# Optimization experiments

Hardware: AMD Instinct MI355X
Metric: run time of the kernel (lower is better)

Reference implementation:

```python
import math
import jax, jax.numpy as jnp
import numpy as np

B, S, H = 8, 1024, 1024
NH = 16
HD = H // NH  # 64


def setup_inputs() -> dict:
    key = jax.random.key(0)
    k1, k2, k3, k4 = jax.random.split(key, 4)
    hidden_states = jax.random.normal(k1, (B, S, H), dtype=jnp.float32)
    attention_mask = jax.random.randint(k2, (B, 1, 1, S), 0, 2, dtype=jnp.int32)
    w_qkv = jax.random.normal(k3, (H, 3 * H), dtype=jnp.float32) * (1.0 / math.sqrt(H))
    b_qkv = jax.random.normal(k4, (3 * H,), dtype=jnp.float32) * 0.02
    return {"hidden_states": hidden_states, "attention_mask": attention_mask,
            "w_qkv": w_qkv, "b_qkv": b_qkv}


def reference(hidden_states, attention_mask, w_qkv, b_qkv):
    b, s, _ = hidden_states.shape
    # fused QKV projection: [b, s, 3H]
    qkv = jnp.einsum('bsh,hk->bsk', hidden_states, w_qkv) + b_qkv
    # view (b, s, nh, 3*hd) -> permute -> chunk last dim (per-head q|k|v layout)
    qkv = qkv.reshape(b, s, NH, 3, HD)
    qkv = jnp.transpose(qkv, (0, 2, 1, 3, 4))      # [b, nh, s, 3, hd]
    q, k, v = qkv[..., 0, :], qkv[..., 1, :], qkv[..., 2, :]
    # raw scores, then FusedScaleMaskSoftmax semantics: scale * scores, mask, fp32 softmax
    scores = jnp.einsum('bhqd,bhkd->bhqk', q, k)
    scale = math.sqrt(HD)  # module passes sqrt(head_dim) as multiplicative scale
    scores = scores.astype(jnp.float32) * scale
    mask = attention_mask != 0                     # nonzero -> masked (padding)
    scores = jnp.where(mask, jnp.float32(-10000.0), scores)
    probs = jax.nn.softmax(scores, axis=-1).astype(hidden_states.dtype)
    # dropout prob = 0 -> identity
    context = jnp.einsum('bhqk,bhkd->bhqd', probs, v)
    context = jnp.transpose(context, (0, 2, 1, 3)).reshape(b, s, NH * HD)
    return context
```

## Files before the change

kernel.cpp:

```cpp
#include <hip/hip_runtime.h>
#include <math.h>

#define Bdim 8
#define Sdim 1024
#define Hdim 1024
#define NHd 16
#define HDd 64
#define N3H 3072

#define Q_OFF   0u
#define K_OFF   16777216u
#define V_OFF   33554432u
#define WH_OFF  41943040u
#define WL_OFF  45088768u
#define AHI_OFF 0u
#define ALO_OFF 8388608u

typedef __bf16 bf16x8 __attribute__((ext_vector_type(8)));
typedef float  f32x4  __attribute__((ext_vector_type(4)));

__device__ __forceinline__ unsigned short f2bf(float x) {
  unsigned b = __builtin_bit_cast(unsigned, x);
  return (unsigned short)((b + 0x7FFFu + ((b >> 16) & 1u)) >> 16);
}
__device__ __forceinline__ float bf2f(unsigned short h) {
  unsigned b = ((unsigned)h) << 16;
  return __builtin_bit_cast(float, b);
}
__device__ __forceinline__ void split_hl(float v, unsigned short& h, unsigned short& l) {
  h = f2bf(v);
  l = f2bf(v - bf2f(h));
}
__device__ __forceinline__ void async16(void* lds, const void* g) {
  __builtin_amdgcn_global_load_lds((const __attribute__((address_space(1))) unsigned int*)g,
                                   (__attribute__((address_space(3))) unsigned int*)lds, 16, 0, 0);
}

__global__ __launch_bounds__(256) void convert_AW(
    const float* __restrict__ A, const float* __restrict__ W,
    unsigned short* __restrict__ aout, unsigned short* __restrict__ ws)
{
  __shared__ float T[64][65];
  const int tid = threadIdx.x;
  int bid = blockIdx.x;
  if (bid < 4096) {
    size_t i = ((size_t)bid * 256 + tid) * 8;
    float4 a0 = *(const float4*)&A[i];
    float4 a1 = *(const float4*)&A[i + 4];
    float av[8] = {a0.x, a0.y, a0.z, a0.w, a1.x, a1.y, a1.z, a1.w};
    unsigned short h[8], l[8];
    #pragma unroll
    for (int j = 0; j < 8; ++j) split_hl(av[j], h[j], l[j]);
    *(uint4*)&aout[AHI_OFF + i] = *(uint4*)h;
    *(uint4*)&aout[ALO_OFF + i] = *(uint4*)l;
    return;
  }
  bid -= 4096;
  const int n0 = (bid % (N3H / 64)) * 64;
  const int k0 = (bid / (N3H / 64)) * 64;
  #pragma unroll
  for (int r = 0; r < 4; ++r) {
    int k = r * 16 + (tid >> 4);
    int n = (tid & 15) * 4;
    float4 v = *(const float4*)&W[(size_t)(k0 + k) * N3H + n0 + n];
    T[k][n + 0] = v.x; T[k][n + 1] = v.y; T[k][n + 2] = v.z; T[k][n + 3] = v.w;
  }
  __syncthreads();
  int n = tid >> 2;
  int kl = (tid & 3) * 16;
  unsigned short h[16], l[16];
  #pragma unroll
  for (int i = 0; i < 16; ++i) split_hl(T[kl + i][n], h[i], l[i]);
  size_t base = (size_t)(n0 + n) * 1024 + k0 + kl;
  *(uint4*)&ws[WH_OFF + base]     = *(uint4*)&h[0];
  *(uint4*)&ws[WH_OFF + base + 8] = *(uint4*)&h[8];
  *(uint4*)&ws[WL_OFF + base]     = *(uint4*)&l[0];
  *(uint4*)&ws[WL_OFF + base + 8] = *(uint4*)&l[8];
}

__global__ __launch_bounds__(256, 2) void qkv_mfma(
    const unsigned short* __restrict__ ao,
    const unsigned short* __restrict__ ws,
    const float* __restrict__ bias,
    unsigned short* __restrict__ wso)
{
  __shared__ unsigned short sA[2][128 * 32];
  __shared__ unsigned short sB[2][128 * 32];

  const int tid  = threadIdx.x;
  const int wave = tid >> 6;
  const int lane = tid & 63;
  const int l16  = lane & 15;
  const int quad = lane >> 4;

  const int n0 = blockIdx.x * 128;
  const int m0 = blockIdx.y * 128;
  const int wm = (wave >> 1) * 64;
  const int wn = (wave & 1) * 64;

  const unsigned short* Ah = ao + AHI_OFF;
  const unsigned short* Al = ao + ALO_OFF;
  const unsigned short* Wh = ws + WH_OFF;
  const unsigned short* Wl = ws + WL_OFF;

  f32x4 acc[4][4];
  #pragma unroll
  for (int i = 0; i < 4; ++i)
    #pragma unroll
    for (int j = 0; j < 4; ++j) acc[i][j] = (f32x4){0.f, 0.f, 0.f, 0.f};

  for (int kt = 0; kt < 1024; kt += 32) {
    __syncthreads();
    #pragma unroll
    for (int r = 0; r < 2; ++r) {
      int chunk = r * 256 + tid;
      int row = chunk >> 2;
      int c8  = (chunk & 3) << 3;
      int ldsoff = (r * 256 + wave * 64) * 8;
      async16(&sA[0][ldsoff], &Ah[(size_t)(m0 + row) * 1024 + kt + c8]);
      async16(&sA[1][ldsoff], &Al[(size_t)(m0 + row) * 1024 + kt + c8]);
      async16(&sB[0][ldsoff], &Wh[(size_t)(n0 + row) * 1024 + kt + c8]);
      async16(&sB[1][ldsoff], &Wl[(size_t)(n0 + row) * 1024 + kt + c8]);
    }
    __syncthreads();

    bf16x8 af[4][2], bf[4][2];
    #pragma unroll
    for (int i = 0; i < 4; ++i) {
      int row = wm + i * 16 + l16;
      af[i][0] = *(const bf16x8*)&sA[0][row * 32 + quad * 8];
      af[i][1] = *(const bf16x8*)&sA[1][row * 32 + quad * 8];
    }
    #pragma unroll
    for (int j = 0; j < 4; ++j) {
      int row = wn + j * 16 + l16;
      bf[j][0] = *(const bf16x8*)&sB[0][row * 32 + quad * 8];
      bf[j][1] = *(const bf16x8*)&sB[1][row * 32 + quad * 8];
    }
    #pragma unroll
    for (int i = 0; i < 4; ++i)
      #pragma unroll
      for (int j = 0; j < 4; ++j) {
        acc[i][j] = __builtin_amdgcn_mfma_f32_16x16x32_bf16(af[i][0], bf[j][0], acc[i][j], 0, 0, 0);
        acc[i][j] = __builtin_amdgcn_mfma_f32_16x16x32_bf16(af[i][1], bf[j][0], acc[i][j], 0, 0, 0);
        acc[i][j] = __builtin_amdgcn_mfma_f32_16x16x32_bf16(af[i][0], bf[j][1], acc[i][j], 0, 0, 0);
      }
  }

  const int ncol0 = n0 + wn;
  const int which = (ncol0 >> 6) % 3;
  const int head  = ncol0 / 192;
  const int mrow0 = m0 + wm;
  const int bb = mrow0 >> 10;
  const int sb = mrow0 & 1023;
  const int bh = bb * NHd + head;

  float bs[4];
  #pragma unroll
  for (int j = 0; j < 4; ++j) bs[j] = bias[ncol0 + j * 16 + l16];

  if (which == 0) {
    unsigned short* dst = wso + Q_OFF + ((size_t)bh * Sdim + sb) * 128;
    #pragma unroll
    for (int i = 0; i < 4; ++i)
      #pragma unroll
      for (int j = 0; j < 4; ++j) {
        int d = j * 16 + l16;
        #pragma unroll
        for (int r = 0; r < 4; ++r) {
          int s = i * 16 + quad * 4 + r;
          unsigned short h, l;
          split_hl(acc[i][j][r] + bs[j], h, l);
          dst[(size_t)s * 128 + d]      = h;
          dst[(size_t)s * 128 + 64 + d] = l;
        }
      }
  } else if (which == 1) {
    unsigned short* dst = wso + K_OFF + (size_t)bh * 131072 + (size_t)(sb >> 6) * 8192;
    #pragma unroll
    for (int i = 0; i < 4; ++i)
      #pragma unroll
      for (int j = 0; j < 4; ++j) {
        int c = j * 16 + l16;
        #pragma unroll
        for (int r = 0; r < 4; ++r) {
          int sp = i * 16 + quad * 4 + r;
          int idx = ((((sp >> 4) * 4 + (c >> 5)) * 64 + ((c >> 3) & 3) * 16 + (sp & 15)) << 3) + (c & 7);
          unsigned short h, l;
          split_hl(acc[i][j][r] + bs[j], h, l);
          dst[idx]        = h;
          dst[idx + 1024] = l;
        }
      }
  } else {
    unsigned short* dst = wso + V_OFF + (size_t)bh * 65536 + (size_t)(sb >> 6) * 4096;
    #pragma unroll
    for (int i = 0; i < 4; ++i)
      #pragma unroll
      for (int j = 0; j < 4; ++j) {
        int dr = j * 16 + l16;
        int ky = i * 16 + quad * 4;
        int idx = ((((dr >> 4) * 2 + (ky >> 5)) * 64 + ((ky >> 3) & 3) * 16 + (dr & 15)) << 3) + (ky & 7);
        unsigned short p[4];
        #pragma unroll
        for (int r = 0; r < 4; ++r) p[r] = f2bf(acc[i][j][r] + bs[j]);
        *(uint2*)&dst[idx] = *(uint2*)p;
      }
  }
}

__global__ __launch_bounds__(256, 4) void attn_mfma(
    const unsigned short* __restrict__ qhl,
    const unsigned short* __restrict__ khl,
    const unsigned short* __restrict__ vt,
    const int* __restrict__ mask,
    float* __restrict__ out)
{
  __shared__ unsigned short Ks[8192];
  __shared__ unsigned short Vs[4096];
  __shared__ unsigned short Pw[4][1024];
  __shared__ float msks[1024];

  const int tid  = threadIdx.x;
  const int wave = tid >> 6;
  const int lane = tid & 63;
  const int l16  = lane & 15;
  const int quad = lane >> 4;

  const int xcd = blockIdx.x & 7;
  const int s_  = blockIdx.x >> 3;
  const int bh  = xcd + ((s_ & 7) << 3) + ((s_ >> 7) << 6);
  const int qt  = (s_ >> 3) & 15;
  const int bb  = bh >> 4;
  const int q0  = qt * 64;

  const unsigned short* kplane = khl + (size_t)bh * 131072;
  const unsigned short* vplane = vt  + (size_t)bh * 65536;

  {
    int4 mv = *(const int4*)&mask[bb * Sdim + tid * 4];
    msks[tid * 4 + 0] = mv.x ? 1.f : 0.f;
    msks[tid * 4 + 1] = mv.y ? 1.f : 0.f;
    msks[tid * 4 + 2] = mv.z ? 1.f : 0.f;
    msks[tid * 4 + 3] = mv.w ? 1.f : 0.f;
  }

  bf16x8 qf[4];
  {
    int row = q0 + wave * 16 + l16;
    const unsigned short* src = qhl + ((size_t)bh * Sdim + row) * 128;
    #pragma unroll
    for (int kk = 0; kk < 4; ++kk)
      qf[kk] = *(const bf16x8*)&src[kk * 32 + quad * 8];
  }

  f32x4 O[4] = {{0.f,0.f,0.f,0.f},{0.f,0.f,0.f,0.f},{0.f,0.f,0.f,0.f},{0.f,0.f,0.f,0.f}};
  float mrow[4] = {-INFINITY, -INFINITY, -INFINITY, -INFINITY};
  float lrow[4] = {0.f, 0.f, 0.f, 0.f};

  #pragma unroll 1
  for (int kt = 0; kt < 16; ++kt) {
    __syncthreads();
    {
      const unsigned short* ksrc = kplane + (size_t)kt * 8192;
      const unsigned short* vsrc = vplane + (size_t)kt * 4096;
      #pragma unroll
      for (int r = 0; r < 4; ++r)
        async16(&Ks[(r * 256 + tid) * 8], &ksrc[(size_t)(r * 256 + tid) * 8]);
      #pragma unroll
      for (int r = 0; r < 2; ++r)
        async16(&Vs[(r * 256 + tid) * 8], &vsrc[(size_t)(r * 256 + tid) * 8]);
    }
    __syncthreads();

    f32x4 sc[4];
    __builtin_amdgcn_s_setprio(1);
    #pragma unroll
    for (int ns = 0; ns < 4; ++ns) {
      f32x4 c = {0.f, 0.f, 0.f, 0.f};
      bf16x8 kf0 = *(const bf16x8*)&Ks[((ns * 4 + 0) * 64 + lane) * 8];
      bf16x8 kf1 = *(const bf16x8*)&Ks[((ns * 4 + 1) * 64 + lane) * 8];
      bf16x8 kf2 = *(const bf16x8*)&Ks[((ns * 4 + 2) * 64 + lane) * 8];
      bf16x8 kf3 = *(const bf16x8*)&Ks[((ns * 4 + 3) * 64 + lane) * 8];
      c = __builtin_amdgcn_mfma_f32_16x16x32_bf16(qf[0], kf0, c, 0, 0, 0);
      c = __builtin_amdgcn_mfma_f32_16x16x32_bf16(qf[1], kf1, c, 0, 0, 0);
      c = __builtin_amdgcn_mfma_f32_16x16x32_bf16(qf[2], kf0, c, 0, 0, 0);
      c = __builtin_amdgcn_mfma_f32_16x16x32_bf16(qf[3], kf1, c, 0, 0, 0);
      c = __builtin_amdgcn_mfma_f32_16x16x32_bf16(qf[0], kf2, c, 0, 0, 0);
      c = __builtin_amdgcn_mfma_f32_16x16x32_bf16(qf[1], kf3, c, 0, 0, 0);
      sc[ns] = c;
    }
    __builtin_amdgcn_s_setprio(0);

    float rmax[4] = {-INFINITY, -INFINITY, -INFINITY, -INFINITY};
    #pragma unroll
    for (int ns = 0; ns < 4; ++ns) {
      float mk = msks[kt * 64 + ns * 16 + l16];
      #pragma unroll
      for (int r = 0; r < 4; ++r) {
        float s = (mk != 0.f) ? -10000.f : sc[ns][r] * 8.f;
        sc[ns][r] = s;
        rmax[r] = fmaxf(rmax[r], s);
      }
    }
    #pragma unroll
    for (int r = 0; r < 4; ++r) {
      float v = rmax[r];
      v = fmaxf(v, __shfl_xor(v, 1, 16));
      v = fmaxf(v, __shfl_xor(v, 2, 16));
      v = fmaxf(v, __shfl_xor(v, 4, 16));
      v = fmaxf(v, __shfl_xor(v, 8, 16));
      rmax[r] = v;
    }

    bool nosk = !(rmax[0] <= mrow[0] + 8.f && rmax[1] <= mrow[1] + 8.f &&
                  rmax[2] <= mrow[2] + 8.f && rmax[3] <= mrow[3] + 8.f);
    if (__any((int)nosk)) {
      float alpha[4];
      #pragma unroll
      for (int r = 0; r < 4; ++r) {
        float mn = fmaxf(mrow[r], rmax[r]);
        alpha[r] = __expf(mrow[r] - mn);
        mrow[r] = mn;
        lrow[r] *= alpha[r];
      }
      #pragma unroll
      for (int d = 0; d < 4; ++d)
        #pragma unroll
        for (int r = 0; r < 4; ++r) O[d][r] *= alpha[r];
    }

    float rsum[4] = {0.f, 0.f, 0.f, 0.f};
    #pragma unroll
    for (int ns = 0; ns < 4; ++ns) {
      int key = ns * 16 + l16;
      int cbase = (((key >> 5) * 4 + ((key >> 3) & 3)) * 16 + quad * 4) * 8 + (key & 7);
      #pragma unroll
      for (int r = 0; r < 4; ++r) {
        float p = __expf(sc[ns][r] - mrow[r]);
        rsum[r] += p;
        Pw[wave][cbase + r * 8] = f2bf(p);
      }
    }
    #pragma unroll
    for (int r = 0; r < 4; ++r) {
      float v = rsum[r];
      v += __shfl_xor(v, 1, 16);
      v += __shfl_xor(v, 2, 16);
      v += __shfl_xor(v, 4, 16);
      v += __shfl_xor(v, 8, 16);
      lrow[r] += v;
    }

    bf16x8 pf[2];
    #pragma unroll
    for (int kk = 0; kk < 2; ++kk)
      pf[kk] = *(const bf16x8*)&Pw[wave][((kk * 4 + quad) * 16 + l16) * 8];
    __builtin_amdgcn_s_setprio(1);
    #pragma unroll
    for (int d = 0; d < 4; ++d)
      #pragma unroll
      for (int kk = 0; kk < 2; ++kk) {
        bf16x8 vf = *(const bf16x8*)&Vs[((d * 2 + kk) * 64 + lane) * 8];
        O[d] = __builtin_amdgcn_mfma_f32_16x16x32_bf16(pf[kk], vf, O[d], 0, 0, 0);
      }
    __builtin_amdgcn_s_setprio(0);
  }

  const int h = bh & 15;
  #pragma unroll
  for (int r = 0; r < 4; ++r) {
    float inv = 1.f / lrow[r];
    int q = q0 + wave * 16 + quad * 4 + r;
    float* dst = out + ((size_t)bb * Sdim + q) * Hdim + h * HDd;
    #pragma unroll
    for (int d = 0; d < 4; ++d)
      dst[d * 16 + l16] = O[d][r] * inv;
  }
}

extern "C" void kernel_launch(void* const* d_in, const int* in_sizes, int n_in,
                              void* d_out, int out_size, void* d_ws, size_t ws_size,
                              hipStream_t stream) {
  const float* hs   = (const float*)d_in[0];
  const int*   mask = (const int*)d_in[1];
  const float* w    = (const float*)d_in[2];
  const float* bias = (const float*)d_in[3];
  float* out = (float*)d_out;
  unsigned short* ws = (unsigned short*)d_ws;
  unsigned short* ao = (unsigned short*)d_out;

  convert_AW<<<4096 + (N3H / 64) * (1024 / 64), 256, 0, stream>>>(hs, w, ao, ws);

  qkv_mfma<<<dim3(N3H / 128, 8192 / 128), 256, 0, stream>>>(ao, ws, bias, ws);

  attn_mfma<<<Bdim * NHd * (Sdim / 64), 256, 0, stream>>>(
      ws + Q_OFF, ws + K_OFF, ws + V_OFF, mask, out);
}
```

Before: 371.2 us.

## Process two 16-row query tiles per wave in attention to reuse K/V tiles

Each attention block now covers 128 query rows instead of 64, with every wave handling two 16-row query sub-tiles that share the K and V fragments loaded from LDS. This halves the number of blocks and the total global-to-LDS K/V traffic, and interleaves independent MFMA chains to hide latency. In exchange it roughly doubles the accumulator and score registers per wave, doubles the P scratch in LDS, lowers the occupancy hint from 4 to 3 blocks, and leaves fewer blocks (1024) to spread across the CUs.

```diff
diff --git a/kernel.cpp b/kernel.cpp
--- a/kernel.cpp
+++ b/kernel.cpp
@@ -209,7 +209,7 @@
   }
 }
 
-__global__ __launch_bounds__(256, 4) void attn_mfma(
+__global__ __launch_bounds__(256, 3) void attn_mfma(
     const unsigned short* __restrict__ qhl,
     const unsigned short* __restrict__ khl,
     const unsigned short* __restrict__ vt,
@@ -218,7 +218,7 @@
 {
   __shared__ unsigned short Ks[8192];
   __shared__ unsigned short Vs[4096];
-  __shared__ unsigned short Pw[4][1024];
+  __shared__ unsigned short Pw[4][2048];
   __shared__ float msks[1024];
 
   const int tid  = threadIdx.x;
@@ -229,10 +229,10 @@
 
   const int xcd = blockIdx.x & 7;
   const int s_  = blockIdx.x >> 3;
-  const int bh  = xcd + ((s_ & 7) << 3) + ((s_ >> 7) << 6);
-  const int qt  = (s_ >> 3) & 15;
+  const int bh  = xcd + ((s_ & 7) << 3) + ((s_ >> 6) << 6);
+  const int qt  = (s_ >> 3) & 7;
   const int bb  = bh >> 4;
-  const int q0  = qt * 64;
+  const int q0  = qt * 128;
 
   const unsigned short* kplane = khl + (size_t)bh * 131072;
   const unsigned short* vplane = vt  + (size_t)bh * 65536;
@@ -245,18 +245,24 @@
     msks[tid * 4 + 3] = mv.w ? 1.f : 0.f;
   }
 
-  bf16x8 qf[4];
+  bf16x8 qfA[4], qfB[4];
   {
-    int row = q0 + wave * 16 + l16;
-    const unsigned short* src = qhl + ((size_t)bh * Sdim + row) * 128;
-    #pragma unroll
-    for (int kk = 0; kk < 4; ++kk)
-      qf[kk] = *(const bf16x8*)&src[kk * 32 + quad * 8];
-  }
-
-  f32x4 O[4] = {{0.f,0.f,0.f,0.f},{0.f,0.f,0.f,0.f},{0.f,0.f,0.f,0.f},{0.f,0.f,0.f,0.f}};
-  float mrow[4] = {-INFINITY, -INFINITY, -INFINITY, -INFINITY};
-  float lrow[4] = {0.f, 0.f, 0.f, 0.f};
+    int rowA = q0 + wave * 32 + l16;
+    const unsigned short* srcA = qhl + ((size_t)bh * Sdim + rowA) * 128;
+    const unsigned short* srcB = srcA + 16 * 128;
+    #pragma unroll
+    for (int kk = 0; kk < 4; ++kk) {
+      qfA[kk] = *(const bf16x8*)&srcA[kk * 32 + quad * 8];
+      qfB[kk] = *(const bf16x8*)&srcB[kk * 32 + quad * 8];
+    }
+  }
+
+  f32x4 OA[4] = {{0.f,0.f,0.f,0.f},{0.f,0.f,0.f,0.f},{0.f,0.f,0.f,0.f},{0.f,0.f,0.f,0.f}};
+  f32x4 OB[4] = {{0.f,0.f,0.f,0.f},{0.f,0.f,0.f,0.f},{0.f,0.f,0.f,0.f},{0.f,0.f,0.f,0.f}};
+  float mrowA[4] = {-INFINITY,-INFINITY,-INFINITY,-INFINITY};
+  float mrowB[4] = {-INFINITY,-INFINITY,-INFINITY,-INFINITY};
+  float lrowA[4] = {0.f,0.f,0.f,0.f};
+  float lrowB[4] = {0.f,0.f,0.f,0.f};
 
   #pragma unroll 1
   for (int kt = 0; kt < 16; ++kt) {
@@ -273,96 +279,111 @@
     }
     __syncthreads();
 
-    f32x4 sc[4];
+    f32x4 scA[4], scB[4];
     __builtin_amdgcn_s_setprio(1);
     #pragma unroll
     for (int ns = 0; ns < 4; ++ns) {
-      f32x4 c = {0.f, 0.f, 0.f, 0.f};
       bf16x8 kf0 = *(const bf16x8*)&Ks[((ns * 4 + 0) * 64 + lane) * 8];
       bf16x8 kf1 = *(const bf16x8*)&Ks[((ns * 4 + 1) * 64 + lane) * 8];
       bf16x8 kf2 = *(const bf16x8*)&Ks[((ns * 4 + 2) * 64 + lane) * 8];
       bf16x8 kf3 = *(const bf16x8*)&Ks[((ns * 4 + 3) * 64 + lane) * 8];
-      c = __builtin_amdgcn_mfma_f32_16x16x32_bf16(qf[0], kf0, c, 0, 0, 0);
-      c = __builtin_amdgcn_mfma_f32_16x16x32_bf16(qf[1], kf1, c, 0, 0, 0);
-      c = __builtin_amdgcn_mfma_f32_16x16x32_bf16(qf[2], kf0, c, 0, 0, 0);
-      c = __builtin_amdgcn_mfma_f32_16x16x32_bf16(qf[3], kf1, c, 0, 0, 0);
-      c = __builtin_amdgcn_mfma_f32_16x16x32_bf16(qf[0], kf2, c, 0, 0, 0);
-      c = __builtin_amdgcn_mfma_f32_16x16x32_bf16(qf[1], kf3, c, 0, 0, 0);
-      sc[ns] = c;
+      f32x4 cA = {0.f,0.f,0.f,0.f}, cB = {0.f,0.f,0.f,0.f};
+      cA = __builtin_amdgcn_mfma_f32_16x16x32_bf16(qfA[0], kf0, cA, 0, 0, 0);
+      cB = __builtin_amdgcn_mfma_f32_16x16x32_bf16(qfB[0], kf0, cB, 0, 0, 0);
+      cA = __builtin_amdgcn_mfma_f32_16x16x32_bf16(qfA[1], kf1, cA, 0, 0, 0);
+      cB = __builtin_amdgcn_mfma_f32_16x16x32_bf16(qfB[1], kf1, cB, 0, 0, 0);
+      cA = __builtin_amdgcn_mfma_f32_16x16x32_bf16(qfA[2], kf0, cA, 0, 0, 0);
+      cB = __builtin_amdgcn_mfma_f32_16x16x32_bf16(qfB[2], kf0, cB, 0, 0, 0);
+      cA = __builtin_amdgcn_mfma_f32_16x16x32_bf16(qfA[3], kf1, cA, 0, 0, 0);
+      cB = __builtin_amdgcn_mfma_f32_16x16x32_bf16(qfB[3], kf1, cB, 0, 0, 0);
+      cA = __builtin_amdgcn_mfma_f32_16x16x32_bf16(qfA[0], kf2, cA, 0, 0, 0);
+      cB = __builtin_amdgcn_mfma_f32_16x16x32_bf16(qfB[0], kf2, cB, 0, 0, 0);
+      cA = __builtin_amdgcn_mfma_f32_16x16x32_bf16(qfA[1], kf3, cA, 0, 0, 0);
+      cB = __builtin_amdgcn_mfma_f32_16x16x32_bf16(qfB[1], kf3, cB, 0, 0, 0);
+      scA[ns] = cA; scB[ns] = cB;
     }
     __builtin_amdgcn_s_setprio(0);
 
-    float rmax[4] = {-INFINITY, -INFINITY, -INFINITY, -INFINITY};
+    float rmaxA[4] = {-INFINITY,-INFINITY,-INFINITY,-INFINITY};
+    float rmaxB[4] = {-INFINITY,-INFINITY,-INFINITY,-INFINITY};
     #pragma unroll
     for (int ns = 0; ns < 4; ++ns) {
       float mk = msks[kt * 64 + ns * 16 + l16];
       #pragma unroll
       for (int r = 0; r < 4; ++r) {
-        float s = (mk != 0.f) ? -10000.f : sc[ns][r] * 8.f;
-        sc[ns][r] = s;
-        rmax[r] = fmaxf(rmax[r], s);
+        float sA2 = (mk != 0.f) ? -10000.f : scA[ns][r] * 8.f;
+        float sB2 = (mk != 0.f) ? -10000.f : scB[ns][r] * 8.f;
+        scA[ns][r] = sA2; scB[ns][r] = sB2;
+        rmaxA[r] = fmaxf(rmaxA[r], sA2);
+        rmaxB[r] = fmaxf(rmaxB[r], sB2);
       }
     }
     #pragma unroll
     for (int r = 0; r < 4; ++r) {
-      float v = rmax[r];
-      v = fmaxf(v, __shfl_xor(v, 1, 16));
-      v = fmaxf(v, __shfl_xor(v, 2, 16));
-      v = fmaxf(v, __shfl_xor(v, 4, 16));
-      v = fmaxf(v, __shfl_xor(v, 8, 16));
-      rmax[r] = v;
-    }
-
-    bool nosk = !(rmax[0] <= mrow[0] + 8.f && rmax[1] <= mrow[1] + 8.f &&
-                  rmax[2] <= mrow[2] + 8.f && rmax[3] <= mrow[3] + 8.f);
+      float vA = rmaxA[r], vB = rmaxB[r];
+      vA = fmaxf(vA, __shfl_xor(vA, 1, 16)); vB = fmaxf(vB, __shfl_xor(vB, 1, 16));
+      vA = fmaxf(vA, __shfl_xor(vA, 2, 16)); vB = fmaxf(vB, __shfl_xor(vB, 2, 16));
+      vA = fmaxf(vA, __shfl_xor(vA, 4, 16)); vB = fmaxf(vB, __shfl_xor(vB, 4, 16));
+      vA = fmaxf(vA, __shfl_xor(vA, 8, 16)); vB = fmaxf(vB, __shfl_xor(vB, 8, 16));
+      rmaxA[r] = vA; rmaxB[r] = vB;
+    }
+
+    bool nosk = !(rmaxA[0] <= mrowA[0] + 8.f && rmaxA[1] <= mrowA[1] + 8.f &&
+                  rmaxA[2] <= mrowA[2] + 8.f && rmaxA[3] <= mrowA[3] + 8.f &&
+                  rmaxB[0] <= mrowB[0] + 8.f && rmaxB[1] <= mrowB[1] + 8.f &&
+                  rmaxB[2] <= mrowB[2] + 8.f && rmaxB[3] <= mrowB[3] + 8.f);
     if (__any((int)nosk)) {
-      float alpha[4];
       #pragma unroll
       for (int r = 0; r < 4; ++r) {
-        float mn = fmaxf(mrow[r], rmax[r]);
-        alpha[r] = __expf(mrow[r] - mn);
-        mrow[r] = mn;
-        lrow[r] *= alpha[r];
-      }
-      #pragma unroll
-      for (int d = 0; d < 4; ++d)
+        float mnA = fmaxf(mrowA[r], rmaxA[r]);
+        float mnB = fmaxf(mrowB[r], rmaxB[r]);
+        float aA = __expf(mrowA[r] - mnA);
+        float aB = __expf(mrowB[r] - mnB);
+        mrowA[r] = mnA; mrowB[r] = mnB;
+        lrowA[r] *= aA;  lrowB[r] *= aB;
         #pragma unroll
-        for (int r = 0; r < 4; ++r) O[d][r] *= alpha[r];
-    }
-
-    float rsum[4] = {0.f, 0.f, 0.f, 0.f};
+        for (int d = 0; d < 4; ++d) { OA[d][r] *= aA; OB[d][r] *= aB; }
+      }
+    }
+
+    float rsumA[4] = {0.f,0.f,0.f,0.f}, rsumB[4] = {0.f,0.f,0.f,0.f};
     #pragma unroll
     for (int ns = 0; ns < 4; ++ns) {
       int key = ns * 16 + l16;
       int cbase = (((key >> 5) * 4 + ((key >> 3) & 3)) * 16 + quad * 4) * 8 + (key & 7);
       #pragma unroll
       for (int r = 0; r < 4; ++r) {
-        float p = __expf(sc[ns][r] - mrow[r]);
-        rsum[r] += p;
-        Pw[wave][cbase + r * 8] = f2bf(p);
+        float pA = __expf(scA[ns][r] - mrowA[r]);
+        float pB = __expf(scB[ns][r] - mrowB[r]);
+        rsumA[r] += pA; rsumB[r] += pB;
+        Pw[wave][cbase + r * 8]        = f2bf(pA);
+        Pw[wave][1024 + cbase + r * 8] = f2bf(pB);
       }
     }
     #pragma unroll
     for (int r = 0; r < 4; ++r) {
-      float v = rsum[r];
-      v += __shfl_xor(v, 1, 16);
-      v += __shfl_xor(v, 2, 16);
-      v += __shfl_xor(v, 4, 16);
-      v += __shfl_xor(v, 8, 16);
-      lrow[r] += v;
-    }
-
-    bf16x8 pf[2];
-    #pragma unroll
-    for (int kk = 0; kk < 2; ++kk)
-      pf[kk] = *(const bf16x8*)&Pw[wave][((kk * 4 + quad) * 16 + l16) * 8];
+      float vA = rsumA[r], vB = rsumB[r];
+      vA += __shfl_xor(vA, 1, 16); vB += __shfl_xor(vB, 1, 16);
+      vA += __shfl_xor(vA, 2, 16); vB += __shfl_xor(vB, 2, 16);
+      vA += __shfl_xor(vA, 4, 16); vB += __shfl_xor(vB, 4, 16);
+      vA += __shfl_xor(vA, 8, 16); vB += __shfl_xor(vB, 8, 16);
+      lrowA[r] += vA; lrowB[r] += vB;
+    }
+
+    bf16x8 pfA[2], pfB[2];
+    #pragma unroll
+    for (int kk = 0; kk < 2; ++kk) {
+      pfA[kk] = *(const bf16x8*)&Pw[wave][((kk * 4 + quad) * 16 + l16) * 8];
+      pfB[kk] = *(const bf16x8*)&Pw[wave][1024 + ((kk * 4 + quad) * 16 + l16) * 8];
+    }
     __builtin_amdgcn_s_setprio(1);
     #pragma unroll
     for (int d = 0; d < 4; ++d)
       #pragma unroll
       for (int kk = 0; kk < 2; ++kk) {
         bf16x8 vf = *(const bf16x8*)&Vs[((d * 2 + kk) * 64 + lane) * 8];
-        O[d] = __builtin_amdgcn_mfma_f32_16x16x32_bf16(pf[kk], vf, O[d], 0, 0, 0);
+        OA[d] = __builtin_amdgcn_mfma_f32_16x16x32_bf16(pfA[kk], vf, OA[d], 0, 0, 0);
+        OB[d] = __builtin_amdgcn_mfma_f32_16x16x32_bf16(pfB[kk], vf, OB[d], 0, 0, 0);
       }
     __builtin_amdgcn_s_setprio(0);
   }
@@ -370,12 +391,16 @@
   const int h = bh & 15;
   #pragma unroll
   for (int r = 0; r < 4; ++r) {
-    float inv = 1.f / lrow[r];
-    int q = q0 + wave * 16 + quad * 4 + r;
-    float* dst = out + ((size_t)bb * Sdim + q) * Hdim + h * HDd;
-    #pragma unroll
-    for (int d = 0; d < 4; ++d)
-      dst[d * 16 + l16] = O[d][r] * inv;
+    float invA = 1.f / lrowA[r];
+    float invB = 1.f / lrowB[r];
+    int qA = q0 + wave * 32 + quad * 4 + r;
+    float* dstA = out + ((size_t)bb * Sdim + qA) * Hdim + h * HDd;
+    float* dstB = dstA + 16 * Hdim;
+    #pragma unroll
+    for (int d = 0; d < 4; ++d) {
+      dstA[d * 16 + l16] = OA[d][r] * invA;
+      dstB[d * 16 + l16] = OB[d][r] * invB;
+    }
   }
 }
 
@@ -394,6 +419,6 @@
 
   qkv_mfma<<<dim3(N3H / 128, 8192 / 128), 256, 0, stream>>>(ao, ws, bias, ws);
 
-  attn_mfma<<<Bdim * NHd * (Sdim / 64), 256, 0, stream>>>(
+  attn_mfma<<<Bdim * NHd * (Sdim / 128), 256, 0, stream>>>(
       ws + Q_OFF, ws + K_OFF, ws + V_OFF, mask, out);
 }
```

After: 367.2 us. About the same (-1.1%).
